# Kernel optimization log

Hardware: AMD Instinct MI355X
Metric: run time of the kernel (lower is better)

The kernel has to match this reference:

```python
import jax, jax.numpy as jnp
import numpy as np

N_NODES = 50000
N_EDGES = 800000
IN_DIM = 256
HID = 128
N_GRAPHS = 64
NEG_SLOPE = 0.2


def _gat_layer(x, src, dst, W, a_src, a_dst, b, n_nodes):
    """Single-head PyG-style GATConv. src/dst already include self-loops."""
    h = x @ W                                   # [N, F]
    alpha_s = h @ a_src                         # [N]
    alpha_d = h @ a_dst                         # [N]
    e = jax.nn.leaky_relu(alpha_s[src] + alpha_d[dst], NEG_SLOPE)  # [E]
    # scatter-softmax over edges grouped by destination node
    m = jax.ops.segment_max(e, dst, num_segments=n_nodes)          # [N]
    w = jnp.exp(e - m[dst])                                        # [E]
    denom = jax.ops.segment_sum(w, dst, num_segments=n_nodes)      # [N] (>0: self-loops)
    coef = w / denom[dst]                                          # [E]
    out = jax.ops.segment_sum(h[src] * coef[:, None], dst, num_segments=n_nodes)
    return out + b


def setup_inputs() -> dict:
    key = jax.random.key(0)
    ks = jax.random.split(key, 12)
    x = jax.random.normal(ks[0], (N_NODES, IN_DIM), dtype=jnp.float32)
    edge_index = jax.random.randint(ks[1], (2, N_EDGES), 0, N_NODES, dtype=jnp.int64)
    batch = jnp.sort(jax.random.randint(ks[2], (N_NODES,), 0, N_GRAPHS, dtype=jnp.int64))
    s1 = 1.0 / np.sqrt(IN_DIM)
    s2 = 1.0 / np.sqrt(HID)
    return {
        "x": x,
        "edge_index": edge_index,
        "batch": batch,
        "W1": jax.random.normal(ks[3], (IN_DIM, HID), dtype=jnp.float32) * s1,
        "a_src1": jax.random.normal(ks[4], (HID,), dtype=jnp.float32) * s2,
        "a_dst1": jax.random.normal(ks[5], (HID,), dtype=jnp.float32) * s2,
        "b1": jnp.zeros((HID,), dtype=jnp.float32),
        "W2": jax.random.normal(ks[6], (HID, HID), dtype=jnp.float32) * s2,
        "a_src2": jax.random.normal(ks[7], (HID,), dtype=jnp.float32) * s2,
        "a_dst2": jax.random.normal(ks[8], (HID,), dtype=jnp.float32) * s2,
        "b2": jnp.zeros((HID,), dtype=jnp.float32),
        "Wc": jax.random.normal(ks[9], (HID, 1), dtype=jnp.float32) * s2,
        "bc": jnp.zeros((1,), dtype=jnp.float32),
    }


def reference(x, edge_index, batch, W1, a_src1, a_dst1, b1, W2, a_src2, a_dst2, b2, Wc, bc):
    n = x.shape[0]
    loops = jnp.arange(n, dtype=edge_index.dtype)
    src = jnp.concatenate([edge_index[0], loops])  # messages flow src -> dst
    dst = jnp.concatenate([edge_index[1], loops])
    h = jax.nn.relu(_gat_layer(x, src, dst, W1, a_src1, a_dst1, b1, n))
    h = jax.nn.relu(_gat_layer(h, src, dst, W2, a_src2, a_dst2, b2, n))
    # global mean pool over graphs
    summed = jax.ops.segment_sum(h, batch, num_segments=N_GRAPHS)          # [G, HID]
    counts = jax.ops.segment_sum(jnp.ones((n,), h.dtype), batch, num_segments=N_GRAPHS)
    pooled = summed / jnp.maximum(counts, 1.0)[:, None]
    return jax.nn.sigmoid(pooled @ Wc + bc)        # [G, 1]
```

## Files before the change

### kernel.cpp

```cpp
#include <hip/hip_runtime.h>
#include <hip/hip_bf16.h>
#include <math.h>

#define N_NODES 50000
#define N_EDGES 800000
#define E_TOT   (N_EDGES + N_NODES)
#define HID     128
#define N_GRAPHS 64
#define NEG_SLOPE 0.2f

#define NBKT 196
#define CAPB 6144
#define CHUNK3 4096
#define NB3  ((E_TOT + CHUNK3 - 1) / CHUNK3)
#define NB_BOUNDS ((N_NODES + 255) / 256)

typedef __attribute__((ext_vector_type(8))) short bf16x8;
typedef __attribute__((ext_vector_type(4))) float f32x4;

__device__ __forceinline__ ushort f2bf(float f) {
    union { float f; uint u; } x; x.f = f;
    uint r = x.u + 0x7fffu + ((x.u >> 16) & 1u);
    return (ushort)(r >> 16);
}
__device__ __forceinline__ float bfbits2f(uint bits_hi) {
    union { uint u; float f; } x; x.u = bits_hi;
    return x.f;
}

__global__ __launch_bounds__(256) void prep(const float* __restrict__ W1,
                                            const float* __restrict__ W2,
                                            ushort* __restrict__ Wt1,
                                            ushort* __restrict__ Wt2,
                                            int* __restrict__ gcur) {
    int idx = blockIdx.x * 256 + threadIdx.x;
    if (idx < 256 * 128) {
        int k = idx >> 7, n = idx & 127;
        Wt1[n * 256 + k] = f2bf(W1[idx]);
    } else if (idx < 256 * 128 + 128 * 128) {
        int j = idx - 256 * 128;
        int k = j >> 7, n = j & 127;
        Wt2[n * 128 + k] = f2bf(W2[j]);
    }
    if (idx <= NBKT) gcur[idx] = 0;
}

__global__ __launch_bounds__(256) void bin_scatter(const int* __restrict__ edge_src,
                                                   const int* __restrict__ edge_dst,
                                                   int* __restrict__ gcur,
                                                   uint* __restrict__ staged) {
    __shared__ int hist[256], scan_s[256], base_l[256], cur[256], runbase[256];
    __shared__ uint vals[CHUNK3];
    int tid = threadIdx.x;
    int e0 = blockIdx.x * CHUNK3;
    int cnt = min(CHUNK3, E_TOT - e0);

    hist[tid] = 0;
    __syncthreads();
    for (int i = tid; i < cnt; i += 256) {
        int e = e0 + i;
        int d = (e < N_EDGES) ? edge_dst[e] : (e - N_EDGES);
        atomicAdd(&hist[d >> 8], 1);
    }
    __syncthreads();
    int v = hist[tid];
    scan_s[tid] = v;
    __syncthreads();
    for (int off = 1; off < 256; off <<= 1) {
        int t = (tid >= off) ? scan_s[tid - off] : 0;
        __syncthreads();
        scan_s[tid] += t;
        __syncthreads();
    }
    base_l[tid] = scan_s[tid] - v;
    cur[tid] = scan_s[tid] - v;
    __syncthreads();
    for (int i = tid; i < cnt; i += 256) {
        int e = e0 + i;
        int s, d;
        if (e < N_EDGES) { s = edge_src[e]; d = edge_dst[e]; }
        else             { s = d = e - N_EDGES; }
        int p = atomicAdd(&cur[d >> 8], 1);
        vals[p] = ((uint)(d >> 8) << 24) | ((uint)s << 8) | (uint)(d & 255);
    }
    __syncthreads();
    if (tid < NBKT && hist[tid] > 0) runbase[tid] = atomicAdd(&gcur[tid], hist[tid]);
    __syncthreads();
    for (int i = tid; i < cnt; i += 256) {
        uint v2 = vals[i];
        int b = (int)(v2 >> 24);
        int idx = runbase[b] + (i - base_l[b]);
        if (idx < CAPB) staged[b * CAPB + idx] = v2;
    }
}

__global__ __launch_bounds__(256) void scan_bounds(const int* __restrict__ gcur,
                                                   int* __restrict__ bbase,
                                                   int* __restrict__ row_start,
                                                   const int* __restrict__ batch,
                                                   int* __restrict__ gstart) {
    int tid = threadIdx.x;
    if (blockIdx.x == NB_BOUNDS) {
        __shared__ int s[256];
        int v = (tid < NBKT) ? gcur[tid] : 0;
        s[tid] = v;
        __syncthreads();
        for (int off = 1; off < 256; off <<= 1) {
            int t = (tid >= off) ? s[tid - off] : 0;
            __syncthreads();
            s[tid] += t;
            __syncthreads();
        }
        if (tid < NBKT) bbase[tid] = s[tid] - v;
        if (tid == 255) { bbase[NBKT] = s[255]; row_start[N_NODES] = s[255]; }
    } else {
        int i = blockIdx.x * 256 + tid;
        if (i >= N_NODES) return;
        int b  = batch[i];
        int bp = (i == 0) ? -1 : batch[i - 1];
        for (int g = bp + 1; g <= b; g++) gstart[g] = i;
        if (i == N_NODES - 1) {
            for (int g = b + 1; g <= N_GRAPHS; g++) gstart[g] = N_NODES;
        }
    }
}

__global__ __launch_bounds__(256) void bucket_build(const uint* __restrict__ staged,
                                                    const int* __restrict__ bbase,
                                                    int* __restrict__ row_start,
                                                    ushort* __restrict__ csr_src) {
    __shared__ int hist[256], scan_s[256], base_l[256];
    __shared__ uint lv[CAPB];
    int tid = threadIdx.x;
    int b = blockIdx.x;
    int base = bbase[b];
    int cnt = bbase[b + 1] - base;

    hist[tid] = 0;
    __syncthreads();
    for (int i = tid; i < cnt; i += 256) {
        uint v = staged[b * CAPB + i];
        lv[i] = v;
        atomicAdd(&hist[v & 255], 1);
    }
    __syncthreads();
    int v0 = hist[tid];
    scan_s[tid] = v0;
    __syncthreads();
    for (int off = 1; off < 256; off <<= 1) {
        int t = (tid >= off) ? scan_s[tid - off] : 0;
        __syncthreads();
        scan_s[tid] += t;
        __syncthreads();
    }
    int excl = scan_s[tid] - v0;
    base_l[tid] = excl;
    int node = b * 256 + tid;
    if (node < N_NODES) row_start[node] = base + excl;
    __syncthreads();
    for (int i = tid; i < cnt; i += 256) {
        uint v = lv[i];
        int pos = base + atomicAdd(&base_l[v & 255], 1);
        csr_src[pos] = (ushort)((v >> 8) & 0xFFFFu);
    }
}

template <int K, bool ABF>
__global__ __launch_bounds__(256) void gemm_mfma(const void* __restrict__ Aptr,
                                                 const ushort* __restrict__ Wt,
                                                 ushort* __restrict__ Cbf,
                                                 const float* __restrict__ a_sv,
                                                 const float* __restrict__ a_dv,
                                                 float* __restrict__ alpha_s,
                                                 float* __restrict__ alpha_d, int M) {
    constexpr int KC = 64;
    constexpr int AP = 72;
    __shared__ ushort As[64 * AP];
    __shared__ ushort Bs[128 * AP];

    int tid = threadIdx.x;
    int lane = tid & 63;
    int wv = tid >> 6;
    int mrow = lane & 15;
    int quad = lane >> 4;
    int row0 = blockIdx.x * 64;

    f32x4 acc[8];
#pragma unroll
    for (int t = 0; t < 8; t++) acc[t] = (f32x4){0.f, 0.f, 0.f, 0.f};

    for (int k0 = 0; k0 < K; k0 += KC) {
        if constexpr (!ABF) {
            const float* A = (const float*)Aptr;
#pragma unroll
            for (int p = 0; p < 2; p++) {
                int c = p * 256 + tid;
                int r = c >> 3;
                int kk = (c & 7) * 8;
                int grow = row0 + r;
                float4 v0 = make_float4(0.f, 0.f, 0.f, 0.f);
                float4 v1 = v0;
                if (grow < M) {
                    const float* src = &A[(size_t)grow * K + k0 + kk];
                    v0 = *(const float4*)src;
                    v1 = *(const float4*)(src + 4);
                }
                uint4 w;
                w.x = (uint)f2bf(v0.x) | ((uint)f2bf(v0.y) << 16);
                w.y = (uint)f2bf(v0.z) | ((uint)f2bf(v0.w) << 16);
                w.z = (uint)f2bf(v1.x) | ((uint)f2bf(v1.y) << 16);
                w.w = (uint)f2bf(v1.z) | ((uint)f2bf(v1.w) << 16);
                *(uint4*)&As[r * AP + kk] = w;
            }
        } else {
            const ushort* A = (const ushort*)Aptr;
#pragma unroll
            for (int p = 0; p < 2; p++) {
                int c = p * 256 + tid;
                int r = c >> 3;
                int kk = (c & 7) * 8;
                int grow = row0 + r;
                uint4 v = make_uint4(0, 0, 0, 0);
                if (grow < M) v = *(const uint4*)&A[(size_t)grow * K + k0 + kk];
                *(uint4*)&As[r * AP + kk] = v;
            }
        }
#pragma unroll
        for (int p = 0; p < 4; p++) {
            int c = p * 256 + tid;
            int n = c >> 3;
            int kk = (c & 7) * 8;
            uint4 v = *(const uint4*)&Wt[(size_t)n * K + k0 + kk];
            *(uint4*)&Bs[n * AP + kk] = v;
        }
        __syncthreads();

        const ushort* arow = &As[(wv * 16 + mrow) * AP + quad * 8];
        const ushort* brow = &Bs[mrow * AP + quad * 8];
#pragma unroll
        for (int ks = 0; ks < KC; ks += 32) {
            bf16x8 a = *(const bf16x8*)&arow[ks];
#pragma unroll
            for (int t = 0; t < 8; t++) {
                bf16x8 b = *(const bf16x8*)&brow[t * 16 * AP + ks];
                acc[t] = __builtin_amdgcn_mfma_f32_16x16x32_bf16(a, b, acc[t], 0, 0, 0);
            }
        }
        __syncthreads();
    }

    float as_r[8], ad_r[8];
#pragma unroll
    for (int t = 0; t < 8; t++) {
        int col = t * 16 + mrow;
        as_r[t] = a_sv[col];
        ad_r[t] = a_dv[col];
    }
#pragma unroll
    for (int r = 0; r < 4; r++) {
        float ps = 0.f, pd = 0.f;
#pragma unroll
        for (int t = 0; t < 8; t++) {
            ps = fmaf(acc[t][r], as_r[t], ps);
            pd = fmaf(acc[t][r], ad_r[t], pd);
        }
#pragma unroll
        for (int o = 1; o < 16; o <<= 1) {
            ps += __shfl_xor(ps, o, 64);
            pd += __shfl_xor(pd, o, 64);
        }
        int row = row0 + wv * 16 + quad * 4 + r;
        if (mrow == 0 && row < M) {
            alpha_s[row] = ps;
            alpha_d[row] = pd;
        }
    }

#pragma unroll
    for (int t = 0; t < 8; t++) {
#pragma unroll
        for (int r = 0; r < 4; r++) {
            int row = row0 + wv * 16 + quad * 4 + r;
            if (row < M)
                Cbf[(size_t)row * HID + t * 16 + mrow] = f2bf(acc[t][r]);
        }
    }
}

__global__ __launch_bounds__(256) void gat_aggregate(const ushort* __restrict__ hbf,
                                                     const float* __restrict__ alpha_s,
                                                     const float* __restrict__ alpha_d,
                                                     const int* __restrict__ row_start,
                                                     const ushort* __restrict__ csr_src,
                                                     const float* __restrict__ bias,
                                                     ushort* __restrict__ outbf) {
    __shared__ float exv[4][4][72];
    __shared__ uint  sov[4][4][72];
    int wv = threadIdx.x >> 6;
    int lane = threadIdx.x & 63;
    int q = lane >> 4;
    int l = lane & 15;
    int n = blockIdx.x * 16 + wv * 4 + q;
    float* exq = exv[wv][q];
    uint*  soq = sov[wv][q];

    int beg = row_start[n];
    int deg = row_start[n + 1] - beg;
    float adn = alpha_d[n];
    int c8 = l * 8;
    const char* hbase = (const char*)hbf + c8 * 2;

    float a[8];
#pragma unroll
    for (int i = 0; i < 8; i++) a[i] = 0.f;
    float ssum = 0.f;

    for (int c0 = 0; c0 < deg; c0 += 64) {
        int cnt = min(64, deg - c0);
        for (int k = l; k < 72; k += 16) {
            if (k < cnt) {
                int s = csr_src[beg + c0 + k];
                float e = alpha_s[s] + adn;
                e = (e > 0.f) ? e : e * NEG_SLOPE;
                float ex = __expf(e);
                exq[k] = ex;
                soq[k] = (uint)s * (HID * 2);
                ssum += ex;
            } else {
                exq[k] = 0.f;
                soq[k] = 0u;
            }
        }
        __builtin_amdgcn_wave_barrier();
        int cm = cnt;
        cm = max(cm, __shfl_xor(cm, 16, 64));
        cm = max(cm, __shfl_xor(cm, 32, 64));
        for (int t0 = 0; t0 < cm; t0 += 8) {
            uint off[8]; uint4 v[8]; float w[8];
#pragma unroll
            for (int b = 0; b < 8; b++) off[b] = soq[t0 + b];
#pragma unroll
            for (int b = 0; b < 8; b++) v[b] = *(const uint4*)(hbase + off[b]);
#pragma unroll
            for (int b = 0; b < 8; b++) w[b] = exq[t0 + b];
#pragma unroll
            for (int b = 0; b < 8; b++) {
                a[0] = fmaf(w[b], bfbits2f(v[b].x << 16), a[0]);
                a[1] = fmaf(w[b], bfbits2f(v[b].x & 0xffff0000u), a[1]);
                a[2] = fmaf(w[b], bfbits2f(v[b].y << 16), a[2]);
                a[3] = fmaf(w[b], bfbits2f(v[b].y & 0xffff0000u), a[3]);
                a[4] = fmaf(w[b], bfbits2f(v[b].z << 16), a[4]);
                a[5] = fmaf(w[b], bfbits2f(v[b].z & 0xffff0000u), a[5]);
                a[6] = fmaf(w[b], bfbits2f(v[b].w << 16), a[6]);
                a[7] = fmaf(w[b], bfbits2f(v[b].w & 0xffff0000u), a[7]);
            }
        }
        __builtin_amdgcn_wave_barrier();
    }

    ssum += __shfl_xor(ssum, 1, 64);
    ssum += __shfl_xor(ssum, 2, 64);
    ssum += __shfl_xor(ssum, 4, 64);
    ssum += __shfl_xor(ssum, 8, 64);
    float inv = 1.f / ssum;
    float4 b0 = *(const float4*)&bias[c8];
    float4 b1 = *(const float4*)&bias[c8 + 4];
    float o0 = fmaxf(fmaf(a[0], inv, b0.x), 0.f);
    float o1 = fmaxf(fmaf(a[1], inv, b0.y), 0.f);
    float o2 = fmaxf(fmaf(a[2], inv, b0.z), 0.f);
    float o3 = fmaxf(fmaf(a[3], inv, b0.w), 0.f);
    float o4 = fmaxf(fmaf(a[4], inv, b1.x), 0.f);
    float o5 = fmaxf(fmaf(a[5], inv, b1.y), 0.f);
    float o6 = fmaxf(fmaf(a[6], inv, b1.z), 0.f);
    float o7 = fmaxf(fmaf(a[7], inv, b1.w), 0.f);
    uint4 pk;
    pk.x = (uint)f2bf(o0) | ((uint)f2bf(o1) << 16);
    pk.y = (uint)f2bf(o2) | ((uint)f2bf(o3) << 16);
    pk.z = (uint)f2bf(o4) | ((uint)f2bf(o5) << 16);
    pk.w = (uint)f2bf(o6) | ((uint)f2bf(o7) << 16);
    *(uint4*)&outbf[(size_t)n * HID + c8] = pk;
}

__global__ __launch_bounds__(128) void pool_partial(const ushort* __restrict__ h,
                                                    const int* __restrict__ gstart,
                                                    float* __restrict__ pool) {
    int g = blockIdx.x;
    int slice = blockIdx.y;
    int d = threadIdx.x;
    int beg = gstart[g], end = gstart[g + 1];
    float acc = 0.f;
    for (int i = beg + slice; i < end; i += 16)
        acc += bfbits2f(((uint)h[(size_t)i * HID + d]) << 16);
    atomicAdd(&pool[g * HID + d], acc);
}

__global__ __launch_bounds__(128) void classify(const float* __restrict__ pool,
                                                const int* __restrict__ gstart,
                                                const float* __restrict__ Wc,
                                                const float* __restrict__ bc,
                                                float* __restrict__ out) {
    int g = blockIdx.x;
    int d = threadIdx.x;
    float cnt = (float)(gstart[g + 1] - gstart[g]);
    float pooled = pool[g * HID + d] / fmaxf(cnt, 1.f);
    float p = pooled * Wc[d];
    __shared__ float red[2];
    for (int o = 32; o; o >>= 1) p += __shfl_xor(p, o, 64);
    if ((d & 63) == 0) red[d >> 6] = p;
    __syncthreads();
    if (d == 0) {
        float t = red[0] + red[1] + bc[0];
        out[g] = 1.f / (1.f + expf(-t));
    }
}

extern "C" void kernel_launch(void* const* d_in, const int* in_sizes, int n_in,
                              void* d_out, int out_size, void* d_ws, size_t ws_size,
                              hipStream_t stream) {
    const float* x     = (const float*)d_in[0];
    const int*   ei    = (const int*)d_in[1];
    const int*   batch = (const int*)d_in[2];
    const float* W1    = (const float*)d_in[3];
    const float* as1   = (const float*)d_in[4];
    const float* ad1   = (const float*)d_in[5];
    const float* b1    = (const float*)d_in[6];
    const float* W2    = (const float*)d_in[7];
    const float* as2   = (const float*)d_in[8];
    const float* ad2   = (const float*)d_in[9];
    const float* b2    = (const float*)d_in[10];
    const float* Wc    = (const float*)d_in[11];
    const float* bc    = (const float*)d_in[12];
    float* out = (float*)d_out;

    char* p = (char*)d_ws;
    auto alloc = [&](size_t bytes) {
        void* r = (void*)p;
        p += (bytes + 255) & ~(size_t)255;
        return r;
    };
    ushort* h0     = (ushort*)alloc((size_t)N_NODES * HID * 2);
    ushort* h1     = (ushort*)alloc((size_t)N_NODES * HID * 2);
    ushort* h2     = (ushort*)alloc((size_t)N_NODES * HID * 2);
    float*  alS    = (float*)alloc((size_t)N_NODES * 4);
    float*  alD    = (float*)alloc((size_t)N_NODES * 4);
    uint*   staged = (uint*)alloc((size_t)NBKT * CAPB * 4);
    ushort* csr    = (ushort*)alloc((size_t)E_TOT * 2);
    int*    rstart = (int*)alloc((size_t)(N_NODES + 1) * 4);
    int*    bbase  = (int*)alloc((NBKT + 1) * 4);
    int*    gcur   = (int*)alloc((NBKT + 1) * 4);
    int*    gstart = (int*)alloc((N_GRAPHS + 1) * 4);
    float*  pool   = (float*)alloc(N_GRAPHS * HID * 4);
    ushort* Wt1    = (ushort*)alloc((size_t)128 * 256 * 2);
    ushort* Wt2    = (ushort*)alloc((size_t)128 * 128 * 2);

    const int* edge_src = ei;
    const int* edge_dst = ei + N_EDGES;

    hipMemsetAsync(pool, 0, (size_t)N_GRAPHS * HID * 4, stream);

    prep<<<192, 256, 0, stream>>>(W1, W2, Wt1, Wt2, gcur);
    bin_scatter<<<NB3, 256, 0, stream>>>(edge_src, edge_dst, gcur, staged);
    scan_bounds<<<NB_BOUNDS + 1, 256, 0, stream>>>(gcur, bbase, rstart, batch, gstart);
    bucket_build<<<NBKT, 256, 0, stream>>>(staged, bbase, rstart, csr);

    gemm_mfma<256, false><<<(N_NODES + 63) / 64, 256, 0, stream>>>(
        x, Wt1, h0, as1, ad1, alS, alD, N_NODES);
    gat_aggregate<<<N_NODES / 16, 256, 0, stream>>>(h0, alS, alD, rstart, csr, b1, h1);

    gemm_mfma<128, true><<<(N_NODES + 63) / 64, 256, 0, stream>>>(
        h1, Wt2, h2, as2, ad2, alS, alD, N_NODES);
    gat_aggregate<<<N_NODES / 16, 256, 0, stream>>>(h2, alS, alD, rstart, csr, b2, h0);

    pool_partial<<<dim3(N_GRAPHS, 16), HID, 0, stream>>>(h0, gstart, pool);
    classify<<<N_GRAPHS, HID, 0, stream>>>(pool, gstart, Wc, bc, out);
}
```

Baseline: 239.2 us.

## Merge preprocessing launches and co-schedule edge binning with first GEMM

Combines weight prep with graph-boundary computation in one launch. The first projection GEMM and the edge bin-scatter now run as disjoint block ranges of a single kernel so they can overlap. The bucket-offset scan moves into each bucket_build block, which drops the separate scan kernel. Pooling writes per-slice partials that classify reduces, removing the memset and the atomics. This cuts launch count and serialization, at the cost of a redundant per-block scan and a larger shared-memory footprint for the fused kernel.

```diff
diff --git a/kernel.cpp b/kernel.cpp
--- a/kernel.cpp
+++ b/kernel.cpp
@@ -13,6 +13,7 @@
 #define CAPB 6144
 #define CHUNK3 4096
 #define NB3  ((E_TOT + CHUNK3 - 1) / CHUNK3)
+#define NBG1 ((N_NODES + 63) / 64)
 #define NB_BOUNDS ((N_NODES + 255) / 256)
 
 typedef __attribute__((ext_vector_type(8))) short bf16x8;
@@ -32,89 +33,25 @@
                                             const float* __restrict__ W2,
                                             ushort* __restrict__ Wt1,
                                             ushort* __restrict__ Wt2,
-                                            int* __restrict__ gcur) {
-    int idx = blockIdx.x * 256 + threadIdx.x;
-    if (idx < 256 * 128) {
-        int k = idx >> 7, n = idx & 127;
-        Wt1[n * 256 + k] = f2bf(W1[idx]);
-    } else if (idx < 256 * 128 + 128 * 128) {
-        int j = idx - 256 * 128;
-        int k = j >> 7, n = j & 127;
-        Wt2[n * 128 + k] = f2bf(W2[j]);
-    }
-    if (idx <= NBKT) gcur[idx] = 0;
-}
-
-__global__ __launch_bounds__(256) void bin_scatter(const int* __restrict__ edge_src,
-                                                   const int* __restrict__ edge_dst,
-                                                   int* __restrict__ gcur,
-                                                   uint* __restrict__ staged) {
-    __shared__ int hist[256], scan_s[256], base_l[256], cur[256], runbase[256];
-    __shared__ uint vals[CHUNK3];
+                                            int* __restrict__ gcur,
+                                            const int* __restrict__ batch,
+                                            int* __restrict__ gstart,
+                                            int* __restrict__ row_start) {
     int tid = threadIdx.x;
-    int e0 = blockIdx.x * CHUNK3;
-    int cnt = min(CHUNK3, E_TOT - e0);
-
-    hist[tid] = 0;
-    __syncthreads();
-    for (int i = tid; i < cnt; i += 256) {
-        int e = e0 + i;
-        int d = (e < N_EDGES) ? edge_dst[e] : (e - N_EDGES);
-        atomicAdd(&hist[d >> 8], 1);
-    }
-    __syncthreads();
-    int v = hist[tid];
-    scan_s[tid] = v;
-    __syncthreads();
-    for (int off = 1; off < 256; off <<= 1) {
-        int t = (tid >= off) ? scan_s[tid - off] : 0;
-        __syncthreads();
-        scan_s[tid] += t;
-        __syncthreads();
-    }
-    base_l[tid] = scan_s[tid] - v;
-    cur[tid] = scan_s[tid] - v;
-    __syncthreads();
-    for (int i = tid; i < cnt; i += 256) {
-        int e = e0 + i;
-        int s, d;
-        if (e < N_EDGES) { s = edge_src[e]; d = edge_dst[e]; }
-        else             { s = d = e - N_EDGES; }
-        int p = atomicAdd(&cur[d >> 8], 1);
-        vals[p] = ((uint)(d >> 8) << 24) | ((uint)s << 8) | (uint)(d & 255);
-    }
-    __syncthreads();
-    if (tid < NBKT && hist[tid] > 0) runbase[tid] = atomicAdd(&gcur[tid], hist[tid]);
-    __syncthreads();
-    for (int i = tid; i < cnt; i += 256) {
-        uint v2 = vals[i];
-        int b = (int)(v2 >> 24);
-        int idx = runbase[b] + (i - base_l[b]);
-        if (idx < CAPB) staged[b * CAPB + idx] = v2;
-    }
-}
-
-__global__ __launch_bounds__(256) void scan_bounds(const int* __restrict__ gcur,
-                                                   int* __restrict__ bbase,
-                                                   int* __restrict__ row_start,
-                                                   const int* __restrict__ batch,
-                                                   int* __restrict__ gstart) {
-    int tid = threadIdx.x;
-    if (blockIdx.x == NB_BOUNDS) {
-        __shared__ int s[256];
-        int v = (tid < NBKT) ? gcur[tid] : 0;
-        s[tid] = v;
-        __syncthreads();
-        for (int off = 1; off < 256; off <<= 1) {
-            int t = (tid >= off) ? s[tid - off] : 0;
-            __syncthreads();
-            s[tid] += t;
-            __syncthreads();
-        }
-        if (tid < NBKT) bbase[tid] = s[tid] - v;
-        if (tid == 255) { bbase[NBKT] = s[255]; row_start[N_NODES] = s[255]; }
+    if (blockIdx.x < 192) {
+        int idx = blockIdx.x * 256 + tid;
+        if (idx < 256 * 128) {
+            int k = idx >> 7, n = idx & 127;
+            Wt1[n * 256 + k] = f2bf(W1[idx]);
+        } else if (idx < 256 * 128 + 128 * 128) {
+            int j = idx - 256 * 128;
+            int k = j >> 7, n = j & 127;
+            Wt2[n * 128 + k] = f2bf(W2[j]);
+        }
+        if (idx <= NBKT) gcur[idx] = 0;
+        if (idx == 0) row_start[N_NODES] = E_TOT;
     } else {
-        int i = blockIdx.x * 256 + tid;
+        int i = (blockIdx.x - 192) * 256 + tid;
         if (i >= N_NODES) return;
         int b  = batch[i];
         int bp = (i == 0) ? -1 : batch[i - 1];
@@ -125,73 +62,36 @@
     }
 }
 
-__global__ __launch_bounds__(256) void bucket_build(const uint* __restrict__ staged,
-                                                    const int* __restrict__ bbase,
-                                                    int* __restrict__ row_start,
-                                                    ushort* __restrict__ csr_src) {
-    __shared__ int hist[256], scan_s[256], base_l[256];
-    __shared__ uint lv[CAPB];
+__global__ __launch_bounds__(256) void gemm1_scatter(const float* __restrict__ A,
+                                                     const ushort* __restrict__ Wt,
+                                                     ushort* __restrict__ Cbf,
+                                                     const float* __restrict__ a_sv,
+                                                     const float* __restrict__ a_dv,
+                                                     float* __restrict__ alpha_s,
+                                                     float* __restrict__ alpha_d,
+                                                     const int* __restrict__ edge_src,
+                                                     const int* __restrict__ edge_dst,
+                                                     int* __restrict__ gcur,
+                                                     uint* __restrict__ staged) {
+    __shared__ char smem[27648];
     int tid = threadIdx.x;
-    int b = blockIdx.x;
-    int base = bbase[b];
-    int cnt = bbase[b + 1] - base;
-
-    hist[tid] = 0;
-    __syncthreads();
-    for (int i = tid; i < cnt; i += 256) {
-        uint v = staged[b * CAPB + i];
-        lv[i] = v;
-        atomicAdd(&hist[v & 255], 1);
-    }
-    __syncthreads();
-    int v0 = hist[tid];
-    scan_s[tid] = v0;
-    __syncthreads();
-    for (int off = 1; off < 256; off <<= 1) {
-        int t = (tid >= off) ? scan_s[tid - off] : 0;
-        __syncthreads();
-        scan_s[tid] += t;
-        __syncthreads();
-    }
-    int excl = scan_s[tid] - v0;
-    base_l[tid] = excl;
-    int node = b * 256 + tid;
-    if (node < N_NODES) row_start[node] = base + excl;
-    __syncthreads();
-    for (int i = tid; i < cnt; i += 256) {
-        uint v = lv[i];
-        int pos = base + atomicAdd(&base_l[v & 255], 1);
-        csr_src[pos] = (ushort)((v >> 8) & 0xFFFFu);
-    }
-}
-
-template <int K, bool ABF>
-__global__ __launch_bounds__(256) void gemm_mfma(const void* __restrict__ Aptr,
-                                                 const ushort* __restrict__ Wt,
-                                                 ushort* __restrict__ Cbf,
-                                                 const float* __restrict__ a_sv,
-                                                 const float* __restrict__ a_dv,
-                                                 float* __restrict__ alpha_s,
-                                                 float* __restrict__ alpha_d, int M) {
-    constexpr int KC = 64;
-    constexpr int AP = 72;
-    __shared__ ushort As[64 * AP];
-    __shared__ ushort Bs[128 * AP];
-
-    int tid = threadIdx.x;
-    int lane = tid & 63;
-    int wv = tid >> 6;
-    int mrow = lane & 15;
-    int quad = lane >> 4;
-    int row0 = blockIdx.x * 64;
-
-    f32x4 acc[8];
-#pragma unroll
-    for (int t = 0; t < 8; t++) acc[t] = (f32x4){0.f, 0.f, 0.f, 0.f};
-
-    for (int k0 = 0; k0 < K; k0 += KC) {
-        if constexpr (!ABF) {
-            const float* A = (const float*)Aptr;
+
+    if (blockIdx.x < NBG1) {
+        constexpr int K = 256, KC = 64, AP = 72;
+        ushort* As = (ushort*)smem;
+        ushort* Bs = (ushort*)(smem + 9216);
+        int lane = tid & 63;
+        int wv = tid >> 6;
+        int mrow = lane & 15;
+        int quad = lane >> 4;
+        int row0 = blockIdx.x * 64;
+        int M = N_NODES;
+
+        f32x4 acc[8];
+#pragma unroll
+        for (int t = 0; t < 8; t++) acc[t] = (f32x4){0.f, 0.f, 0.f, 0.f};
+
+        for (int k0 = 0; k0 < K; k0 += KC) {
 #pragma unroll
             for (int p = 0; p < 2; p++) {
                 int c = p * 256 + tid;
@@ -212,18 +112,201 @@
                 w.w = (uint)f2bf(v1.z) | ((uint)f2bf(v1.w) << 16);
                 *(uint4*)&As[r * AP + kk] = w;
             }
-        } else {
-            const ushort* A = (const ushort*)Aptr;
-#pragma unroll
-            for (int p = 0; p < 2; p++) {
+#pragma unroll
+            for (int p = 0; p < 4; p++) {
                 int c = p * 256 + tid;
-                int r = c >> 3;
+                int n = c >> 3;
                 int kk = (c & 7) * 8;
-                int grow = row0 + r;
-                uint4 v = make_uint4(0, 0, 0, 0);
-                if (grow < M) v = *(const uint4*)&A[(size_t)grow * K + k0 + kk];
-                *(uint4*)&As[r * AP + kk] = v;
-            }
+                uint4 v = *(const uint4*)&Wt[(size_t)n * K + k0 + kk];
+                *(uint4*)&Bs[n * AP + kk] = v;
+            }
+            __syncthreads();
+
+            const ushort* arow = &As[(wv * 16 + mrow) * AP + quad * 8];
+            const ushort* brow = &Bs[mrow * AP + quad * 8];
+#pragma unroll
+            for (int ks = 0; ks < KC; ks += 32) {
+                bf16x8 a = *(const bf16x8*)&arow[ks];
+#pragma unroll
+                for (int t = 0; t < 8; t++) {
+                    bf16x8 b = *(const bf16x8*)&brow[t * 16 * AP + ks];
+                    acc[t] = __builtin_amdgcn_mfma_f32_16x16x32_bf16(a, b, acc[t], 0, 0, 0);
+                }
+            }
+            __syncthreads();
+        }
+
+        float as_r[8], ad_r[8];
+#pragma unroll
+        for (int t = 0; t < 8; t++) {
+            int col = t * 16 + mrow;
+            as_r[t] = a_sv[col];
+            ad_r[t] = a_dv[col];
+        }
+#pragma unroll
+        for (int r = 0; r < 4; r++) {
+            float ps = 0.f, pd = 0.f;
+#pragma unroll
+            for (int t = 0; t < 8; t++) {
+                ps = fmaf(acc[t][r], as_r[t], ps);
+                pd = fmaf(acc[t][r], ad_r[t], pd);
+            }
+#pragma unroll
+            for (int o = 1; o < 16; o <<= 1) {
+                ps += __shfl_xor(ps, o, 64);
+                pd += __shfl_xor(pd, o, 64);
+            }
+            int row = row0 + wv * 16 + quad * 4 + r;
+            if (mrow == 0 && row < M) {
+                alpha_s[row] = ps;
+                alpha_d[row] = pd;
+            }
+        }
+#pragma unroll
+        for (int t = 0; t < 8; t++) {
+#pragma unroll
+            for (int r = 0; r < 4; r++) {
+                int row = row0 + wv * 16 + quad * 4 + r;
+                if (row < M)
+                    Cbf[(size_t)row * HID + t * 16 + mrow] = f2bf(acc[t][r]);
+            }
+        }
+    } else {
+        int* hist    = (int*)smem;
+        int* scan_s  = hist + 256;
+        int* base_l  = scan_s + 256;
+        int* cur     = base_l + 256;
+        int* runbase = cur + 256;
+        uint* vals   = (uint*)(runbase + 256);
+
+        int e0 = (blockIdx.x - NBG1) * CHUNK3;
+        int cnt = min(CHUNK3, E_TOT - e0);
+
+        hist[tid] = 0;
+        __syncthreads();
+        for (int i = tid; i < cnt; i += 256) {
+            int e = e0 + i;
+            int d = (e < N_EDGES) ? edge_dst[e] : (e - N_EDGES);
+            atomicAdd(&hist[d >> 8], 1);
+        }
+        __syncthreads();
+        int v = hist[tid];
+        scan_s[tid] = v;
+        __syncthreads();
+        for (int off = 1; off < 256; off <<= 1) {
+            int t = (tid >= off) ? scan_s[tid - off] : 0;
+            __syncthreads();
+            scan_s[tid] += t;
+            __syncthreads();
+        }
+        base_l[tid] = scan_s[tid] - v;
+        cur[tid] = scan_s[tid] - v;
+        __syncthreads();
+        for (int i = tid; i < cnt; i += 256) {
+            int e = e0 + i;
+            int s, d;
+            if (e < N_EDGES) { s = edge_src[e]; d = edge_dst[e]; }
+            else             { s = d = e - N_EDGES; }
+            int p = atomicAdd(&cur[d >> 8], 1);
+            vals[p] = ((uint)(d >> 8) << 24) | ((uint)s << 8) | (uint)(d & 255);
+        }
+        __syncthreads();
+        if (tid < NBKT && hist[tid] > 0) runbase[tid] = atomicAdd(&gcur[tid], hist[tid]);
+        __syncthreads();
+        for (int i = tid; i < cnt; i += 256) {
+            uint v2 = vals[i];
+            int b = (int)(v2 >> 24);
+            int idx = runbase[b] + (i - base_l[b]);
+            if (idx < CAPB) staged[b * CAPB + idx] = v2;
+        }
+    }
+}
+
+__global__ __launch_bounds__(256) void bucket_build(const uint* __restrict__ staged,
+                                                    const int* __restrict__ gcur,
+                                                    int* __restrict__ row_start,
+                                                    ushort* __restrict__ csr_src) {
+    __shared__ int hist[256], scan_s[256], base_l[256];
+    __shared__ int sBase, sCnt;
+    __shared__ uint lv[CAPB];
+    int tid = threadIdx.x;
+    int b = blockIdx.x;
+
+    int v = (tid < NBKT) ? min(gcur[tid], CAPB) : 0;
+    scan_s[tid] = v;
+    __syncthreads();
+    for (int off = 1; off < 256; off <<= 1) {
+        int t = (tid >= off) ? scan_s[tid - off] : 0;
+        __syncthreads();
+        scan_s[tid] += t;
+        __syncthreads();
+    }
+    if (tid == b) { sBase = scan_s[tid] - v; sCnt = v; }
+    __syncthreads();
+    int base = sBase;
+    int cnt = sCnt;
+
+    hist[tid] = 0;
+    __syncthreads();
+    for (int i = tid; i < cnt; i += 256) {
+        uint v2 = staged[b * CAPB + i];
+        lv[i] = v2;
+        atomicAdd(&hist[v2 & 255], 1);
+    }
+    __syncthreads();
+    int v0 = hist[tid];
+    scan_s[tid] = v0;
+    __syncthreads();
+    for (int off = 1; off < 256; off <<= 1) {
+        int t = (tid >= off) ? scan_s[tid - off] : 0;
+        __syncthreads();
+        scan_s[tid] += t;
+        __syncthreads();
+    }
+    int excl = scan_s[tid] - v0;
+    base_l[tid] = excl;
+    int node = b * 256 + tid;
+    if (node < N_NODES) row_start[node] = base + excl;
+    __syncthreads();
+    for (int i = tid; i < cnt; i += 256) {
+        uint v2 = lv[i];
+        int pos = base + atomicAdd(&base_l[v2 & 255], 1);
+        csr_src[pos] = (ushort)((v2 >> 8) & 0xFFFFu);
+    }
+}
+
+__global__ __launch_bounds__(256) void gemm_mfma2(const ushort* __restrict__ A,
+                                                  const ushort* __restrict__ Wt,
+                                                  ushort* __restrict__ Cbf,
+                                                  const float* __restrict__ a_sv,
+                                                  const float* __restrict__ a_dv,
+                                                  float* __restrict__ alpha_s,
+                                                  float* __restrict__ alpha_d) {
+    constexpr int K = 128, KC = 64, AP = 72;
+    __shared__ ushort As[64 * AP];
+    __shared__ ushort Bs[128 * AP];
+    int tid = threadIdx.x;
+    int lane = tid & 63;
+    int wv = tid >> 6;
+    int mrow = lane & 15;
+    int quad = lane >> 4;
+    int row0 = blockIdx.x * 64;
+    int M = N_NODES;
+
+    f32x4 acc[8];
+#pragma unroll
+    for (int t = 0; t < 8; t++) acc[t] = (f32x4){0.f, 0.f, 0.f, 0.f};
+
+    for (int k0 = 0; k0 < K; k0 += KC) {
+#pragma unroll
+        for (int p = 0; p < 2; p++) {
+            int c = p * 256 + tid;
+            int r = c >> 3;
+            int kk = (c & 7) * 8;
+            int grow = row0 + r;
+            uint4 v = make_uint4(0, 0, 0, 0);
+            if (grow < M) v = *(const uint4*)&A[(size_t)grow * K + k0 + kk];
+            *(uint4*)&As[r * AP + kk] = v;
         }
 #pragma unroll
         for (int p = 0; p < 4; p++) {
@@ -275,7 +358,6 @@
             alpha_d[row] = pd;
         }
     }
-
 #pragma unroll
     for (int t = 0; t < 8; t++) {
 #pragma unroll
@@ -383,7 +465,7 @@
 
 __global__ __launch_bounds__(128) void pool_partial(const ushort* __restrict__ h,
                                                     const int* __restrict__ gstart,
-                                                    float* __restrict__ pool) {
+                                                    float* __restrict__ pool_p) {
     int g = blockIdx.x;
     int slice = blockIdx.y;
     int d = threadIdx.x;
@@ -391,19 +473,22 @@
     float acc = 0.f;
     for (int i = beg + slice; i < end; i += 16)
         acc += bfbits2f(((uint)h[(size_t)i * HID + d]) << 16);
-    atomicAdd(&pool[g * HID + d], acc);
-}
-
-__global__ __launch_bounds__(128) void classify(const float* __restrict__ pool,
+    pool_p[(g * 16 + slice) * HID + d] = acc;
+}
+
+__global__ __launch_bounds__(128) void classify(const float* __restrict__ pool_p,
                                                 const int* __restrict__ gstart,
                                                 const float* __restrict__ Wc,
                                                 const float* __restrict__ bc,
                                                 float* __restrict__ out) {
     int g = blockIdx.x;
     int d = threadIdx.x;
+    float s = 0.f;
+#pragma unroll
+    for (int sl = 0; sl < 16; sl++)
+        s += pool_p[(g * 16 + sl) * HID + d];
     float cnt = (float)(gstart[g + 1] - gstart[g]);
-    float pooled = pool[g * HID + d] / fmaxf(cnt, 1.f);
-    float p = pooled * Wc[d];
+    float p = (s / fmaxf(cnt, 1.f)) * Wc[d];
     __shared__ float red[2];
     for (int o = 32; o; o >>= 1) p += __shfl_xor(p, o, 64);
     if ((d & 63) == 0) red[d >> 6] = p;
@@ -446,31 +531,22 @@
     uint*   staged = (uint*)alloc((size_t)NBKT * CAPB * 4);
     ushort* csr    = (ushort*)alloc((size_t)E_TOT * 2);
     int*    rstart = (int*)alloc((size_t)(N_NODES + 1) * 4);
-    int*    bbase  = (int*)alloc((NBKT + 1) * 4);
     int*    gcur   = (int*)alloc((NBKT + 1) * 4);
     int*    gstart = (int*)alloc((N_GRAPHS + 1) * 4);
-    float*  pool   = (float*)alloc(N_GRAPHS * HID * 4);
+    float*  pool_p = (float*)alloc((size_t)N_GRAPHS * 16 * HID * 4);
     ushort* Wt1    = (ushort*)alloc((size_t)128 * 256 * 2);
     ushort* Wt2    = (ushort*)alloc((size_t)128 * 128 * 2);
 
     const int* edge_src = ei;
     const int* edge_dst = ei + N_EDGES;
 
-    hipMemsetAsync(pool, 0, (size_t)N_GRAPHS * HID * 4, stream);
-
-    prep<<<192, 256, 0, stream>>>(W1, W2, Wt1, Wt2, gcur);
-    bin_scatter<<<NB3, 256, 0, stream>>>(edge_src, edge_dst, gcur, staged);
-    scan_bounds<<<NB_BOUNDS + 1, 256, 0, stream>>>(gcur, bbase, rstart, batch, gstart);
-    bucket_build<<<NBKT, 256, 0, stream>>>(staged, bbase, rstart, csr);
-
-    gemm_mfma<256, false><<<(N_NODES + 63) / 64, 256, 0, stream>>>(
-        x, Wt1, h0, as1, ad1, alS, alD, N_NODES);
+    prep<<<388, 256, 0, stream>>>(W1, W2, Wt1, Wt2, gcur, batch, gstart, rstart);
+    gemm1_scatter<<<NBG1 + NB3, 256, 0, stream>>>(
+        x, Wt1, h0, as1, ad1, alS, alD, edge_src, edge_dst, gcur, staged);
+    bucket_build<<<NBKT, 256, 0, stream>>>(staged, gcur, rstart, csr);
     gat_aggregate<<<N_NODES / 16, 256, 0, stream>>>(h0, alS, alD, rstart, csr, b1, h1);
-
-    gemm_mfma<128, true><<<(N_NODES + 63) / 64, 256, 0, stream>>>(
-        h1, Wt2, h2, as2, ad2, alS, alD, N_NODES);
+    gemm_mfma2<<<NBG1, 256, 0, stream>>>(h1, Wt2, h2, as2, ad2, alS, alD);
     gat_aggregate<<<N_NODES / 16, 256, 0, stream>>>(h2, alS, alD, rstart, csr, b2, h0);
-
-    pool_partial<<<dim3(N_GRAPHS, 16), HID, 0, stream>>>(h0, gstart, pool);
-    classify<<<N_GRAPHS, HID, 0, stream>>>(pool, gstart, Wc, bc, out);
-}
+    pool_partial<<<dim3(N_GRAPHS, 16), HID, 0, stream>>>(h0, gstart, pool_p);
+    classify<<<N_GRAPHS, HID, 0, stream>>>(pool_p, gstart, Wc, bc, out);
+}
```

Result: faster. 222.7 us (-6.9%).
